# Optimization experiments

Measured on AMD Instinct MI355X. Metric: run time of the kernel, lower is better.

## Reference

```python
import jax, jax.numpy as jnp
import numpy as np

N, G, NPG = 8192, 128, 64        # total nodes, graphs, nodes per graph
D_IN, H, D_OUT = 128, 128, 10
DEG = 16                          # avg degree -> E = N*DEG
K = int(NPG * 0.5)                # keep_ratio = 0.5 -> topk per graph


def setup_inputs() -> dict:
    key = jax.random.key(0)
    ks = jax.random.split(key, 20)
    E = N * DEG
    # within-graph random edges (graphs are contiguous blocks of NPG nodes)
    src = jax.random.randint(ks[0], (E,), 0, NPG)
    dst = jax.random.randint(ks[1], (E,), 0, NPG)
    offs = jnp.repeat(jnp.arange(G, dtype=jnp.int32) * NPG, NPG * DEG)
    edge_index = jnp.stack([src.astype(jnp.int32) + offs, dst.astype(jnp.int32) + offs])
    batch = jnp.repeat(jnp.arange(G, dtype=jnp.int32), NPG)
    x = jax.random.normal(ks[2], (N, D_IN), jnp.float32)

    def lin(k, i, o):
        return jax.random.normal(k, (i, o), jnp.float32) * (1.0 / np.sqrt(i))

    return {
        "x": x, "edge_index": edge_index, "batch": batch,
        "W1": lin(ks[3], D_IN, H), "b1": jnp.zeros((H,), jnp.float32),
        "W2": lin(ks[4], H, H),    "b2": jnp.zeros((H,), jnp.float32),
        "W3": lin(ks[5], H, H),    "b3": jnp.zeros((H,), jnp.float32),
        "Wa": lin(ks[6], 3 * H, 1), "ba": jnp.zeros((1,), jnp.float32),
        "M1": lin(ks[7], 6 * H, H),      "c1": jnp.zeros((H,), jnp.float32),
        "M2": lin(ks[8], H, H // 2),     "c2": jnp.zeros((H // 2,), jnp.float32),
        "M3": lin(ks[9], H // 2, D_OUT), "c3": jnp.zeros((D_OUT,), jnp.float32),
    }


def reference(x, edge_index, batch, W1, b1, W2, b2, W3, b3, Wa, ba,
              M1, c1, M2, c2, M3, c3):
    n = x.shape[0]
    # generate_adjacency: dense [N,N] from edge list (symmetrized)
    A = jnp.zeros((n, n), x.dtype).at[edge_index[0], edge_index[1]].set(1.0)
    A = jnp.maximum(A, A.T)
    # normalize_adjacency: D^{-1/2} (A + I) D^{-1/2}
    A = A + jnp.eye(n, dtype=x.dtype)
    dinv = jax.lax.rsqrt(A.sum(axis=1))
    A = A * dinv[:, None] * dinv[None, :]

    gcn = lambda X, W, b: A @ (X @ W) + b
    h1 = jax.nn.relu(gcn(x, W1, b1))
    h2 = jax.nn.relu(gcn(h1, W2, b2))
    h3 = jax.nn.relu(gcn(h2, W3, b3))
    feats = jnp.concatenate([h1, h2, h3], axis=1)          # [N, 3H]

    # SelfAttentionPooling: GCN attention score + tanh + per-graph topk
    score = jnp.tanh((A @ (feats @ Wa) + ba)[:, 0])        # [N]
    s = score.reshape(G, NPG)                              # [G, NPG]
    _, idx = jax.lax.top_k(s, K)                           # [G, K]
    fg = feats.reshape(G, NPG, 3 * H)
    sel = jnp.take_along_axis(fg, idx[..., None], axis=1)  # [G, K, 3H]
    ssel = jnp.take_along_axis(s, idx, axis=1)             # [G, K]
    masked = sel * ssel[..., None]

    # Readout: mean || max per graph -> [G, 6H]
    readout = jnp.concatenate([masked.mean(axis=1), masked.max(axis=1)], axis=1)

    # MLP (dropout inactive at inference)
    h = jax.nn.relu(readout @ M1 + c1)
    h = jax.nn.relu(h @ M2 + c2)
    return h @ M3 + c3                                     # [G, D_OUT]
```

## Files before the change

kernel.cpp:

```cpp
#include <hip/hip_runtime.h>


#define NGRAPH 128
#define EPG    1024
#define ETOT   131072
#define DIM    128
#define KSEL   32
#define SA     68
#define SH     132

#define OFF_A   0
#define OFF_W   (64*SA)
#define OFF_T   (OFF_W + 16*DIM)
#define OFF_H1  (OFF_T  + 64*SH)
#define OFF_H2  (OFF_H1 + 64*SH)
#define OFF_H3  (OFF_H2 + 64*SH)
#define OFF_PRE (OFF_H3 + 64*SH)
#define OFF_SC  (OFF_PRE + 64)
#define OFF_SEL (OFF_SC + 64)
#define LDS_FLOATS (OFF_SEL + 64)
#define LDS_BYTES  (LDS_FLOATS * 4)

#define FMA8(A, xs, w0, w1) do { \
  A[0] += (xs)*(w0).x; A[1] += (xs)*(w0).y; A[2] += (xs)*(w0).z; A[3] += (xs)*(w0).w; \
  A[4] += (xs)*(w1).x; A[5] += (xs)*(w1).y; A[6] += (xs)*(w1).z; A[7] += (xs)*(w1).w; } while(0)

__device__ __forceinline__ void gcn_layer(float* lds, const float* IN, float* OUT,
                                          const float* __restrict__ Wg,
                                          const float* __restrict__ bg,
                                          const float* __restrict__ waCol, int tid)
{
  float* sW  = lds + OFF_W;
  float* sT  = lds + OFF_T;
  float* sA  = lds + OFF_A;
  float* pre = lds + OFF_PRE;
  const int rq = tid >> 4;
  const int cb = tid & 15;
  const int r0 = rq * 4;
  const int c0 = cb * 8;

  float acc[4][8];
  #pragma unroll
  for (int rr = 0; rr < 4; ++rr)
    #pragma unroll
    for (int cc = 0; cc < 8; ++cc) acc[rr][cc] = 0.f;

  for (int kc = 0; kc < 8; ++kc) {
    {
      const float4* wsrc = (const float4*)(Wg + kc * 16 * DIM);
      float4* wdst = (float4*)sW;
      wdst[tid]       = wsrc[tid];
      wdst[tid + 256] = wsrc[tid + 256];
    }
    __syncthreads();
    #pragma unroll
    for (int kt = 0; kt < 4; ++kt) {
      const int kl = kt * 4;
      const int kg = kc * 16 + kl;
      float4 xv[4];
      #pragma unroll
      for (int rr = 0; rr < 4; ++rr)
        xv[rr] = *(const float4*)&IN[(r0 + rr) * SH + kg];
      float4 w0[4], w1[4];
      #pragma unroll
      for (int i = 0; i < 4; ++i) {
        w0[i] = *(const float4*)&sW[(kl + i) * DIM + c0];
        w1[i] = *(const float4*)&sW[(kl + i) * DIM + c0 + 4];
      }
      #pragma unroll
      for (int rr = 0; rr < 4; ++rr) {
        FMA8(acc[rr], xv[rr].x, w0[0], w1[0]);
        FMA8(acc[rr], xv[rr].y, w0[1], w1[1]);
        FMA8(acc[rr], xv[rr].z, w0[2], w1[2]);
        FMA8(acc[rr], xv[rr].w, w0[3], w1[3]);
      }
    }
    __syncthreads();
  }
  #pragma unroll
  for (int rr = 0; rr < 4; ++rr) {
    float4 t0 = make_float4(acc[rr][0], acc[rr][1], acc[rr][2], acc[rr][3]);
    float4 t1 = make_float4(acc[rr][4], acc[rr][5], acc[rr][6], acc[rr][7]);
    *(float4*)&sT[(r0 + rr) * SH + c0]     = t0;
    *(float4*)&sT[(r0 + rr) * SH + c0 + 4] = t1;
  }
  __syncthreads();

  float4 bv0 = *(const float4*)&bg[c0];
  float4 bv1 = *(const float4*)&bg[c0 + 4];
  float a2[4][8];
  #pragma unroll
  for (int rr = 0; rr < 4; ++rr) {
    a2[rr][0] = bv0.x; a2[rr][1] = bv0.y; a2[rr][2] = bv0.z; a2[rr][3] = bv0.w;
    a2[rr][4] = bv1.x; a2[rr][5] = bv1.y; a2[rr][6] = bv1.z; a2[rr][7] = bv1.w;
  }
  for (int j = 0; j < 64; j += 4) {
    float4 av[4];
    #pragma unroll
    for (int rr = 0; rr < 4; ++rr)
      av[rr] = *(const float4*)&sA[(r0 + rr) * SA + j];
    float4 t0[4], t1[4];
    #pragma unroll
    for (int jj = 0; jj < 4; ++jj) {
      t0[jj] = *(const float4*)&sT[(j + jj) * SH + c0];
      t1[jj] = *(const float4*)&sT[(j + jj) * SH + c0 + 4];
    }
    #pragma unroll
    for (int rr = 0; rr < 4; ++rr) {
      FMA8(a2[rr], av[rr].x, t0[0], t1[0]);
      FMA8(a2[rr], av[rr].y, t0[1], t1[1]);
      FMA8(a2[rr], av[rr].z, t0[2], t1[2]);
      FMA8(a2[rr], av[rr].w, t0[3], t1[3]);
    }
  }
  float4 wa0 = *(const float4*)&waCol[c0];
  float4 wa1 = *(const float4*)&waCol[c0 + 4];
  float pp[4];
  #pragma unroll
  for (int rr = 0; rr < 4; ++rr) {
    float4 o0, o1;
    o0.x = fmaxf(a2[rr][0], 0.f); o0.y = fmaxf(a2[rr][1], 0.f);
    o0.z = fmaxf(a2[rr][2], 0.f); o0.w = fmaxf(a2[rr][3], 0.f);
    o1.x = fmaxf(a2[rr][4], 0.f); o1.y = fmaxf(a2[rr][5], 0.f);
    o1.z = fmaxf(a2[rr][6], 0.f); o1.w = fmaxf(a2[rr][7], 0.f);
    *(float4*)&OUT[(r0 + rr) * SH + c0]     = o0;
    *(float4*)&OUT[(r0 + rr) * SH + c0 + 4] = o1;
    pp[rr] = o0.x*wa0.x + o0.y*wa0.y + o0.z*wa0.z + o0.w*wa0.w
           + o1.x*wa1.x + o1.y*wa1.y + o1.z*wa1.z + o1.w*wa1.w;
  }
  #pragma unroll
  for (int rr = 0; rr < 4; ++rr) {
    pp[rr] += __shfl_xor(pp[rr], 1);
    pp[rr] += __shfl_xor(pp[rr], 2);
    pp[rr] += __shfl_xor(pp[rr], 4);
    pp[rr] += __shfl_xor(pp[rr], 8);
  }
  if ((tid & 15) == 0) {
    #pragma unroll
    for (int rr = 0; rr < 4; ++rr) pre[r0 + rr] += pp[rr];
  }
  __syncthreads();
}

extern "C" __global__ void __launch_bounds__(256, 1)
sagpool(const float* __restrict__ x,  const int* __restrict__ ei,
        const float* __restrict__ W1, const float* __restrict__ b1,
        const float* __restrict__ W2, const float* __restrict__ b2,
        const float* __restrict__ W3, const float* __restrict__ b3,
        const float* __restrict__ Wa, const float* __restrict__ ba,
        const float* __restrict__ M1, const float* __restrict__ c1,
        const float* __restrict__ M2, const float* __restrict__ c2,
        const float* __restrict__ M3, const float* __restrict__ c3,
        float* __restrict__ out)
{
  extern __shared__ float lds[];
  const int g   = blockIdx.x;
  const int tid = threadIdx.x;
  float* sA  = lds + OFF_A;
  float* pre = lds + OFF_PRE;
  float* sc  = lds + OFF_SC;
  float* sel = lds + OFF_SEL;

  for (int i = tid; i < 64 * SA; i += 256) sA[i] = 0.f;
  if (tid < 64) pre[tid] = 0.f;
  __syncthreads();
  {
    const int* srcp = ei + g * EPG;
    const int* dstp = ei + ETOT + g * EPG;
    #pragma unroll
    for (int t = 0; t < 4; ++t) {
      int e = tid + t * 256;
      int s = srcp[e] & 63;
      int d = dstp[e] & 63;
      sA[s * SA + d] = 1.0f;
      sA[d * SA + s] = 1.0f;
    }
  }
  __syncthreads();
  if (tid < 64) sA[tid * SA + tid] += 1.0f;
  __syncthreads();
  {
    int r = tid >> 2, q = tid & 3;
    float sum = 0.f;
    int jb = q * 16;
    #pragma unroll
    for (int j = 0; j < 16; ++j) sum += sA[r * SA + jb + j];
    sum += __shfl_xor(sum, 1);
    sum += __shfl_xor(sum, 2);
    if (q == 0) sc[r] = 1.0f / sqrtf(sum);
  }
  __syncthreads();
  for (int i = tid; i < 4096; i += 256) {
    int r = i >> 6, c = i & 63;
    sA[r * SA + c] *= sc[r] * sc[c];
  }
  {
    const float4* xg = (const float4*)(x + g * 64 * DIM);
    float* h3 = lds + OFF_H3;
    for (int i = tid; i < 2048; i += 256) {
      int r = i >> 5, c4 = i & 31;
      *(float4*)&h3[r * SH + c4 * 4] = xg[i];
    }
  }
  __syncthreads();

  gcn_layer(lds, lds + OFF_H3, lds + OFF_H1, W1, b1, Wa + 0,   tid);
  gcn_layer(lds, lds + OFF_H1, lds + OFF_H2, W2, b2, Wa + 128, tid);
  gcn_layer(lds, lds + OFF_H2, lds + OFF_H3, W3, b3, Wa + 256, tid);

  {
    int r = tid >> 2, q = tid & 3;
    float partial = 0.f;
    int jb = q * 16;
    #pragma unroll
    for (int j = 0; j < 16; ++j) partial += sA[r * SA + jb + j] * pre[jb + j];
    partial += __shfl_xor(partial, 1);
    partial += __shfl_xor(partial, 2);
    if (q == 0) sc[r] = tanhf(partial + ba[0]);
  }
  __syncthreads();

  if (tid < 64) {
    float mys = sc[tid];
    int cnt = 0;
    for (int j = 0; j < 64; ++j) {
      float sj = sc[j];
      cnt += (sj > mys || (sj == mys && j < tid)) ? 1 : 0;
    }
    sel[tid] = (cnt < KSEL) ? 1.0f : 0.0f;
  }
  __syncthreads();

  float* ro  = lds + OFF_T;
  float* mh  = lds + OFF_T + 768;
  float* hm  = lds + OFF_T + 1024;
  float* h2m = lds + OFF_T + 1152;
  for (int c = tid; c < 384; c += 256) {
    int which = c >> 7, cc = c & 127;
    const float* buf = (which == 0) ? (lds + OFF_H1)
                     : (which == 1) ? (lds + OFF_H2) : (lds + OFF_H3);
    float sum = 0.f, mx = -1e30f;
    for (int i = 0; i < 64; ++i) {
      if (sel[i] > 0.5f) {
        float v = sc[i] * buf[i * SH + cc];
        sum += v;
        mx = fmaxf(mx, v);
      }
    }
    ro[c]       = sum * (1.0f / KSEL);
    ro[384 + c] = mx;
  }
  __syncthreads();

  {
    int j = tid & 127, half = tid >> 7;
    float acc = 0.f;
    int k0 = half * 384;
    for (int k = k0; k < k0 + 384; k += 4) {
      float4 r4 = *(const float4*)&ro[k];
      acc += r4.x * M1[(k + 0) * DIM + j];
      acc += r4.y * M1[(k + 1) * DIM + j];
      acc += r4.z * M1[(k + 2) * DIM + j];
      acc += r4.w * M1[(k + 3) * DIM + j];
    }
    mh[half * 128 + j] = acc;
  }
  __syncthreads();
  if (tid < 128) hm[tid] = fmaxf(mh[tid] + mh[128 + tid] + c1[tid], 0.f);
  __syncthreads();
  if (tid < 64) {
    float acc = c2[tid];
    for (int k = 0; k < 128; ++k) acc += hm[k] * M2[k * 64 + tid];
    h2m[tid] = fmaxf(acc, 0.f);
  }
  __syncthreads();
  if (tid < 10) {
    float acc = c3[tid];
    for (int k = 0; k < 64; ++k) acc += h2m[k] * M3[k * 10 + tid];
    out[g * 10 + tid] = acc;
  }
}

extern "C" void kernel_launch(void* const* d_in, const int* in_sizes, int n_in,
                              void* d_out, int out_size, void* d_ws, size_t ws_size,
                              hipStream_t stream) {
  const float* x  = (const float*)d_in[0];
  const int*   ei = (const int*)d_in[1];
  const float* W1 = (const float*)d_in[3];
  const float* b1 = (const float*)d_in[4];
  const float* W2 = (const float*)d_in[5];
  const float* b2 = (const float*)d_in[6];
  const float* W3 = (const float*)d_in[7];
  const float* b3 = (const float*)d_in[8];
  const float* Wa = (const float*)d_in[9];
  const float* ba = (const float*)d_in[10];
  const float* M1 = (const float*)d_in[11];
  const float* c1 = (const float*)d_in[12];
  const float* M2 = (const float*)d_in[13];
  const float* c2 = (const float*)d_in[14];
  const float* M3 = (const float*)d_in[15];
  const float* c3 = (const float*)d_in[16];
  float* out = (float*)d_out;

  (void)hipFuncSetAttribute(reinterpret_cast<const void*>(sagpool),
                            hipFuncAttributeMaxDynamicSharedMemorySize, LDS_BYTES);
  sagpool<<<NGRAPH, 256, LDS_BYTES, stream>>>(x, ei, W1, b1, W2, b2, W3, b3,
                                              Wa, ba, M1, c1, M2, c2, M3, c3, out);
}
```

Before: 157.6 us.

## Split monolithic per-graph kernel into multi-kernel pipeline with half-graph blocks

Replaces the single 128-block kernel with five launches: adjacency build plus X@W1 in parallel blocks, three fused GCN-layer kernels that each use two blocks per graph (32 rows each) and also compute the next layer's H@W, and a final pooling/MLP kernel. The intent is to fill more of the GPU's compute units than 128 blocks can and to shrink per-block LDS so more work runs concurrently. In exchange it adds launch overhead and round trips of intermediates through global workspace memory, and it applies a swizzled LDS layout to reduce bank conflicts.

```diff
diff --git a/kernel.cpp b/kernel.cpp
--- a/kernel.cpp
+++ b/kernel.cpp
@@ -7,164 +7,38 @@
 #define DIM    128
 #define KSEL   32
 #define SA     68
-#define SH     132
-
-#define OFF_A   0
-#define OFF_W   (64*SA)
-#define OFF_T   (OFF_W + 16*DIM)
-#define OFF_H1  (OFF_T  + 64*SH)
-#define OFF_H2  (OFF_H1 + 64*SH)
-#define OFF_H3  (OFF_H2 + 64*SH)
-#define OFF_PRE (OFF_H3 + 64*SH)
-#define OFF_SC  (OFF_PRE + 64)
-#define OFF_SEL (OFF_SC + 64)
-#define LDS_FLOATS (OFF_SEL + 64)
-#define LDS_BYTES  (LDS_FLOATS * 4)
+
+#define WS_A   0
+#define WS_T1  524288
+#define WS_T2  (WS_T1 + 1048576)
+#define WS_H1  (WS_T2 + 1048576)
+#define WS_H2  (WS_H1 + 1048576)
+#define WS_H3  (WS_H2 + 1048576)
+#define WS_PRE (WS_H3 + 1048576)
+#define WS_T3  WS_T1
+
+__device__ __forceinline__ int swoff(int k, int o) {
+  return k * 140 + o * 8 + ((o >> 2) << 2);
+}
 
 #define FMA8(A, xs, w0, w1) do { \
   A[0] += (xs)*(w0).x; A[1] += (xs)*(w0).y; A[2] += (xs)*(w0).z; A[3] += (xs)*(w0).w; \
   A[4] += (xs)*(w1).x; A[5] += (xs)*(w1).y; A[6] += (xs)*(w1).z; A[7] += (xs)*(w1).w; } while(0)
 
-__device__ __forceinline__ void gcn_layer(float* lds, const float* IN, float* OUT,
-                                          const float* __restrict__ Wg,
-                                          const float* __restrict__ bg,
-                                          const float* __restrict__ waCol, int tid)
+__global__ void __launch_bounds__(256, 1)
+k_adj_xw(const int* __restrict__ ei, const float* __restrict__ x,
+         const float* __restrict__ W1, float* __restrict__ wsA,
+         float* __restrict__ T1)
 {
-  float* sW  = lds + OFF_W;
-  float* sT  = lds + OFF_T;
-  float* sA  = lds + OFF_A;
-  float* pre = lds + OFF_PRE;
-  const int rq = tid >> 4;
-  const int cb = tid & 15;
-  const int r0 = rq * 4;
-  const int c0 = cb * 8;
-
-  float acc[4][8];
-  #pragma unroll
-  for (int rr = 0; rr < 4; ++rr)
-    #pragma unroll
-    for (int cc = 0; cc < 8; ++cc) acc[rr][cc] = 0.f;
-
-  for (int kc = 0; kc < 8; ++kc) {
-    {
-      const float4* wsrc = (const float4*)(Wg + kc * 16 * DIM);
-      float4* wdst = (float4*)sW;
-      wdst[tid]       = wsrc[tid];
-      wdst[tid + 256] = wsrc[tid + 256];
-    }
+  __shared__ float smem[6464];
+  const int tid = threadIdx.x;
+
+  if (blockIdx.x < NGRAPH) {
+    const int g = blockIdx.x;
+    float* sA = smem;
+    float* dv = smem + 64 * SA;
+    for (int i = tid; i < 64 * SA; i += 256) sA[i] = 0.f;
     __syncthreads();
-    #pragma unroll
-    for (int kt = 0; kt < 4; ++kt) {
-      const int kl = kt * 4;
-      const int kg = kc * 16 + kl;
-      float4 xv[4];
-      #pragma unroll
-      for (int rr = 0; rr < 4; ++rr)
-        xv[rr] = *(const float4*)&IN[(r0 + rr) * SH + kg];
-      float4 w0[4], w1[4];
-      #pragma unroll
-      for (int i = 0; i < 4; ++i) {
-        w0[i] = *(const float4*)&sW[(kl + i) * DIM + c0];
-        w1[i] = *(const float4*)&sW[(kl + i) * DIM + c0 + 4];
-      }
-      #pragma unroll
-      for (int rr = 0; rr < 4; ++rr) {
-        FMA8(acc[rr], xv[rr].x, w0[0], w1[0]);
-        FMA8(acc[rr], xv[rr].y, w0[1], w1[1]);
-        FMA8(acc[rr], xv[rr].z, w0[2], w1[2]);
-        FMA8(acc[rr], xv[rr].w, w0[3], w1[3]);
-      }
-    }
-    __syncthreads();
-  }
-  #pragma unroll
-  for (int rr = 0; rr < 4; ++rr) {
-    float4 t0 = make_float4(acc[rr][0], acc[rr][1], acc[rr][2], acc[rr][3]);
-    float4 t1 = make_float4(acc[rr][4], acc[rr][5], acc[rr][6], acc[rr][7]);
-    *(float4*)&sT[(r0 + rr) * SH + c0]     = t0;
-    *(float4*)&sT[(r0 + rr) * SH + c0 + 4] = t1;
-  }
-  __syncthreads();
-
-  float4 bv0 = *(const float4*)&bg[c0];
-  float4 bv1 = *(const float4*)&bg[c0 + 4];
-  float a2[4][8];
-  #pragma unroll
-  for (int rr = 0; rr < 4; ++rr) {
-    a2[rr][0] = bv0.x; a2[rr][1] = bv0.y; a2[rr][2] = bv0.z; a2[rr][3] = bv0.w;
-    a2[rr][4] = bv1.x; a2[rr][5] = bv1.y; a2[rr][6] = bv1.z; a2[rr][7] = bv1.w;
-  }
-  for (int j = 0; j < 64; j += 4) {
-    float4 av[4];
-    #pragma unroll
-    for (int rr = 0; rr < 4; ++rr)
-      av[rr] = *(const float4*)&sA[(r0 + rr) * SA + j];
-    float4 t0[4], t1[4];
-    #pragma unroll
-    for (int jj = 0; jj < 4; ++jj) {
-      t0[jj] = *(const float4*)&sT[(j + jj) * SH + c0];
-      t1[jj] = *(const float4*)&sT[(j + jj) * SH + c0 + 4];
-    }
-    #pragma unroll
-    for (int rr = 0; rr < 4; ++rr) {
-      FMA8(a2[rr], av[rr].x, t0[0], t1[0]);
-      FMA8(a2[rr], av[rr].y, t0[1], t1[1]);
-      FMA8(a2[rr], av[rr].z, t0[2], t1[2]);
-      FMA8(a2[rr], av[rr].w, t0[3], t1[3]);
-    }
-  }
-  float4 wa0 = *(const float4*)&waCol[c0];
-  float4 wa1 = *(const float4*)&waCol[c0 + 4];
-  float pp[4];
-  #pragma unroll
-  for (int rr = 0; rr < 4; ++rr) {
-    float4 o0, o1;
-    o0.x = fmaxf(a2[rr][0], 0.f); o0.y = fmaxf(a2[rr][1], 0.f);
-    o0.z = fmaxf(a2[rr][2], 0.f); o0.w = fmaxf(a2[rr][3], 0.f);
-    o1.x = fmaxf(a2[rr][4], 0.f); o1.y = fmaxf(a2[rr][5], 0.f);
-    o1.z = fmaxf(a2[rr][6], 0.f); o1.w = fmaxf(a2[rr][7], 0.f);
-    *(float4*)&OUT[(r0 + rr) * SH + c0]     = o0;
-    *(float4*)&OUT[(r0 + rr) * SH + c0 + 4] = o1;
-    pp[rr] = o0.x*wa0.x + o0.y*wa0.y + o0.z*wa0.z + o0.w*wa0.w
-           + o1.x*wa1.x + o1.y*wa1.y + o1.z*wa1.z + o1.w*wa1.w;
-  }
-  #pragma unroll
-  for (int rr = 0; rr < 4; ++rr) {
-    pp[rr] += __shfl_xor(pp[rr], 1);
-    pp[rr] += __shfl_xor(pp[rr], 2);
-    pp[rr] += __shfl_xor(pp[rr], 4);
-    pp[rr] += __shfl_xor(pp[rr], 8);
-  }
-  if ((tid & 15) == 0) {
-    #pragma unroll
-    for (int rr = 0; rr < 4; ++rr) pre[r0 + rr] += pp[rr];
-  }
-  __syncthreads();
-}
-
-extern "C" __global__ void __launch_bounds__(256, 1)
-sagpool(const float* __restrict__ x,  const int* __restrict__ ei,
-        const float* __restrict__ W1, const float* __restrict__ b1,
-        const float* __restrict__ W2, const float* __restrict__ b2,
-        const float* __restrict__ W3, const float* __restrict__ b3,
-        const float* __restrict__ Wa, const float* __restrict__ ba,
-        const float* __restrict__ M1, const float* __restrict__ c1,
-        const float* __restrict__ M2, const float* __restrict__ c2,
-        const float* __restrict__ M3, const float* __restrict__ c3,
-        float* __restrict__ out)
-{
-  extern __shared__ float lds[];
-  const int g   = blockIdx.x;
-  const int tid = threadIdx.x;
-  float* sA  = lds + OFF_A;
-  float* pre = lds + OFF_PRE;
-  float* sc  = lds + OFF_SC;
-  float* sel = lds + OFF_SEL;
-
-  for (int i = tid; i < 64 * SA; i += 256) sA[i] = 0.f;
-  if (tid < 64) pre[tid] = 0.f;
-  __syncthreads();
-  {
     const int* srcp = ei + g * EPG;
     const int* dstp = ei + ETOT + g * EPG;
     #pragma unroll
@@ -175,74 +49,262 @@
       sA[s * SA + d] = 1.0f;
       sA[d * SA + s] = 1.0f;
     }
-  }
-  __syncthreads();
-  if (tid < 64) sA[tid * SA + tid] += 1.0f;
+    __syncthreads();
+    if (tid < 64) sA[tid * SA + tid] += 1.0f;
+    __syncthreads();
+    {
+      int r = tid >> 2, q = tid & 3;
+      float sum = 0.f;
+      int jb = q * 16;
+      #pragma unroll
+      for (int j = 0; j < 16; ++j) sum += sA[r * SA + jb + j];
+      sum += __shfl_xor(sum, 1);
+      sum += __shfl_xor(sum, 2);
+      if (q == 0) dv[r] = 1.0f / sqrtf(sum);
+    }
+    __syncthreads();
+    float* outA = wsA + g * 4096;
+    for (int i = tid; i < 4096; i += 256) {
+      int r = i >> 6, c = i & 63;
+      outA[i] = sA[r * SA + c] * dv[r] * dv[c];
+    }
+  } else {
+    const int row0 = (blockIdx.x - NGRAPH) * 32;
+    float* sX = smem;
+    float* sW = smem + 4224;
+    {
+      const float4* src = (const float4*)(x + row0 * DIM);
+      for (int i = tid; i < 1024; i += 256) {
+        int r = i >> 5, q = i & 31;
+        *(float4*)&sX[r * 132 + q * 4] = src[i];
+      }
+    }
+    const int rg = tid >> 4, cg = tid & 15;
+    const int r0 = rg * 2, c0 = cg * 8;
+    float acc[2][8];
+    #pragma unroll
+    for (int rr = 0; rr < 2; ++rr)
+      #pragma unroll
+      for (int cc = 0; cc < 8; ++cc) acc[rr][cc] = 0.f;
+
+    for (int kc = 0; kc < 8; ++kc) {
+      __syncthreads();
+      const float4* wsrc = (const float4*)(W1 + kc * 16 * DIM);
+      for (int i = tid; i < 512; i += 256) {
+        int k = i >> 5, q = i & 31;
+        *(float4*)&sW[swoff(k, q >> 1) + (q & 1) * 4] = wsrc[i];
+      }
+      __syncthreads();
+      #pragma unroll
+      for (int kq = 0; kq < 4; ++kq) {
+        const int kk = kq * 4, kg = kc * 16 + kk;
+        float4 x0 = *(const float4*)&sX[r0 * 132 + kg];
+        float4 x1 = *(const float4*)&sX[(r0 + 1) * 132 + kg];
+        float4 w0[4], w1[4];
+        #pragma unroll
+        for (int j = 0; j < 4; ++j) {
+          int base = swoff(kk + j, cg);
+          w0[j] = *(const float4*)&sW[base];
+          w1[j] = *(const float4*)&sW[base + 4];
+        }
+        FMA8(acc[0], x0.x, w0[0], w1[0]); FMA8(acc[0], x0.y, w0[1], w1[1]);
+        FMA8(acc[0], x0.z, w0[2], w1[2]); FMA8(acc[0], x0.w, w0[3], w1[3]);
+        FMA8(acc[1], x1.x, w0[0], w1[0]); FMA8(acc[1], x1.y, w0[1], w1[1]);
+        FMA8(acc[1], x1.z, w0[2], w1[2]); FMA8(acc[1], x1.w, w0[3], w1[3]);
+      }
+    }
+    #pragma unroll
+    for (int rr = 0; rr < 2; ++rr) {
+      float4 t0 = make_float4(acc[rr][0], acc[rr][1], acc[rr][2], acc[rr][3]);
+      float4 t1 = make_float4(acc[rr][4], acc[rr][5], acc[rr][6], acc[rr][7]);
+      *(float4*)&T1[(row0 + r0 + rr) * DIM + c0]     = t0;
+      *(float4*)&T1[(row0 + r0 + rr) * DIM + c0 + 4] = t1;
+    }
+  }
+}
+
+#define FOFF_A 8960
+#define FOFF_H 11136
+#define FOFF_W 15360
+#define FUSED_LDS_FLOATS 17600
+#define FUSED_LDS_BYTES (FUSED_LDS_FLOATS * 4)
+
+__global__ void __launch_bounds__(256, 1)
+k_fused(const float* __restrict__ Tin, const float* __restrict__ wsA,
+        const float* __restrict__ bg, const float* __restrict__ waCol,
+        const float* __restrict__ Wn, float* __restrict__ Hout,
+        float* __restrict__ Tout, float* __restrict__ pre,
+        const int first, const int do_xw)
+{
+  extern __shared__ float lds[];
+  float* sT  = lds;
+  float* sAl = lds + FOFF_A;
+  float* sh  = lds + FOFF_H;
+  float* sW  = lds + FOFF_W;
+  const int tid = threadIdx.x;
+  const int g = blockIdx.x >> 1;
+  const int rbase = (blockIdx.x & 1) * 32;
+  const int growbase = g * 64 + rbase;
+
+  {
+    const float4* src = (const float4*)(Tin + g * 64 * DIM);
+    for (int i = tid; i < 2048; i += 256) {
+      int k = i >> 5, q = i & 31;
+      *(float4*)&sT[swoff(k, q >> 1) + (q & 1) * 4] = src[i];
+    }
+    const float* asrc = wsA + g * 4096 + rbase * 64;
+    for (int i = tid; i < 2048; i += 256)
+      sAl[(i >> 6) * SA + (i & 63)] = asrc[i];
+  }
+  __syncthreads();
+
+  const int rg = tid >> 4, cg = tid & 15;
+  const int r0 = rg * 2, c0 = cg * 8;
+
+  float4 bv0 = *(const float4*)&bg[c0];
+  float4 bv1 = *(const float4*)&bg[c0 + 4];
+  float acc[2][8];
+  #pragma unroll
+  for (int rr = 0; rr < 2; ++rr) {
+    acc[rr][0] = bv0.x; acc[rr][1] = bv0.y; acc[rr][2] = bv0.z; acc[rr][3] = bv0.w;
+    acc[rr][4] = bv1.x; acc[rr][5] = bv1.y; acc[rr][6] = bv1.z; acc[rr][7] = bv1.w;
+  }
+  #pragma unroll
+  for (int kq = 0; kq < 16; ++kq) {
+    const int kk = kq * 4;
+    float4 a0 = *(const float4*)&sAl[r0 * SA + kk];
+    float4 a1 = *(const float4*)&sAl[(r0 + 1) * SA + kk];
+    float4 t0[4], t1[4];
+    #pragma unroll
+    for (int j = 0; j < 4; ++j) {
+      int base = swoff(kk + j, cg);
+      t0[j] = *(const float4*)&sT[base];
+      t1[j] = *(const float4*)&sT[base + 4];
+    }
+    FMA8(acc[0], a0.x, t0[0], t1[0]); FMA8(acc[0], a0.y, t0[1], t1[1]);
+    FMA8(acc[0], a0.z, t0[2], t1[2]); FMA8(acc[0], a0.w, t0[3], t1[3]);
+    FMA8(acc[1], a1.x, t0[0], t1[0]); FMA8(acc[1], a1.y, t0[1], t1[1]);
+    FMA8(acc[1], a1.z, t0[2], t1[2]); FMA8(acc[1], a1.w, t0[3], t1[3]);
+  }
+  float4 wa0 = *(const float4*)&waCol[c0];
+  float4 wa1 = *(const float4*)&waCol[c0 + 4];
+  float pp[2];
+  #pragma unroll
+  for (int rr = 0; rr < 2; ++rr) {
+    float4 o0, o1;
+    o0.x = fmaxf(acc[rr][0], 0.f); o0.y = fmaxf(acc[rr][1], 0.f);
+    o0.z = fmaxf(acc[rr][2], 0.f); o0.w = fmaxf(acc[rr][3], 0.f);
+    o1.x = fmaxf(acc[rr][4], 0.f); o1.y = fmaxf(acc[rr][5], 0.f);
+    o1.z = fmaxf(acc[rr][6], 0.f); o1.w = fmaxf(acc[rr][7], 0.f);
+    *(float4*)&sh[(r0 + rr) * 132 + c0]     = o0;
+    *(float4*)&sh[(r0 + rr) * 132 + c0 + 4] = o1;
+    *(float4*)&Hout[(growbase + r0 + rr) * DIM + c0]     = o0;
+    *(float4*)&Hout[(growbase + r0 + rr) * DIM + c0 + 4] = o1;
+    pp[rr] = o0.x*wa0.x + o0.y*wa0.y + o0.z*wa0.z + o0.w*wa0.w
+           + o1.x*wa1.x + o1.y*wa1.y + o1.z*wa1.z + o1.w*wa1.w;
+  }
+  #pragma unroll
+  for (int rr = 0; rr < 2; ++rr) {
+    pp[rr] += __shfl_xor(pp[rr], 1);
+    pp[rr] += __shfl_xor(pp[rr], 2);
+    pp[rr] += __shfl_xor(pp[rr], 4);
+    pp[rr] += __shfl_xor(pp[rr], 8);
+  }
+  if (cg == 0) {
+    #pragma unroll
+    for (int rr = 0; rr < 2; ++rr) {
+      int row = growbase + r0 + rr;
+      if (first) pre[row] = pp[rr];
+      else       pre[row] += pp[rr];
+    }
+  }
+
+  if (do_xw) {
+    float acc2[2][8];
+    #pragma unroll
+    for (int rr = 0; rr < 2; ++rr)
+      #pragma unroll
+      for (int cc = 0; cc < 8; ++cc) acc2[rr][cc] = 0.f;
+    for (int kc = 0; kc < 8; ++kc) {
+      __syncthreads();
+      const float4* wsrc = (const float4*)(Wn + kc * 16 * DIM);
+      for (int i = tid; i < 512; i += 256) {
+        int k = i >> 5, q = i & 31;
+        *(float4*)&sW[swoff(k, q >> 1) + (q & 1) * 4] = wsrc[i];
+      }
+      __syncthreads();
+      #pragma unroll
+      for (int kq = 0; kq < 4; ++kq) {
+        const int kk = kq * 4, kg = kc * 16 + kk;
+        float4 h0 = *(const float4*)&sh[r0 * 132 + kg];
+        float4 h1 = *(const float4*)&sh[(r0 + 1) * 132 + kg];
+        float4 w0[4], w1[4];
+        #pragma unroll
+        for (int j = 0; j < 4; ++j) {
+          int base = swoff(kk + j, cg);
+          w0[j] = *(const float4*)&sW[base];
+          w1[j] = *(const float4*)&sW[base + 4];
+        }
+        FMA8(acc2[0], h0.x, w0[0], w1[0]); FMA8(acc2[0], h0.y, w0[1], w1[1]);
+        FMA8(acc2[0], h0.z, w0[2], w1[2]); FMA8(acc2[0], h0.w, w0[3], w1[3]);
+        FMA8(acc2[1], h1.x, w0[0], w1[0]); FMA8(acc2[1], h1.y, w0[1], w1[1]);
+        FMA8(acc2[1], h1.z, w0[2], w1[2]); FMA8(acc2[1], h1.w, w0[3], w1[3]);
+      }
+    }
+    #pragma unroll
+    for (int rr = 0; rr < 2; ++rr) {
+      float4 t0 = make_float4(acc2[rr][0], acc2[rr][1], acc2[rr][2], acc2[rr][3]);
+      float4 t1 = make_float4(acc2[rr][4], acc2[rr][5], acc2[rr][6], acc2[rr][7]);
+      *(float4*)&Tout[(growbase + r0 + rr) * DIM + c0]     = t0;
+      *(float4*)&Tout[(growbase + r0 + rr) * DIM + c0 + 4] = t1;
+    }
+  }
+}
+
+__global__ void __launch_bounds__(256, 1)
+k_final(const float* __restrict__ wsA, const float* __restrict__ pre,
+        const float* __restrict__ h1g, const float* __restrict__ h2g,
+        const float* __restrict__ h3g, const float* __restrict__ ba,
+        const float* __restrict__ M1, const float* __restrict__ c1,
+        const float* __restrict__ M2, const float* __restrict__ c2,
+        const float* __restrict__ M3, const float* __restrict__ c3,
+        float* __restrict__ out)
+{
+  __shared__ float spre[64], ssc[64], ssel[64];
+  __shared__ float ro[768], mh[256], hm[128], h2m[64];
+  const int g = blockIdx.x, tid = threadIdx.x;
+
+  if (tid < 64) spre[tid] = pre[g * 64 + tid];
   __syncthreads();
   {
     int r = tid >> 2, q = tid & 3;
-    float sum = 0.f;
-    int jb = q * 16;
-    #pragma unroll
-    for (int j = 0; j < 16; ++j) sum += sA[r * SA + jb + j];
-    sum += __shfl_xor(sum, 1);
-    sum += __shfl_xor(sum, 2);
-    if (q == 0) sc[r] = 1.0f / sqrtf(sum);
-  }
-  __syncthreads();
-  for (int i = tid; i < 4096; i += 256) {
-    int r = i >> 6, c = i & 63;
-    sA[r * SA + c] *= sc[r] * sc[c];
-  }
-  {
-    const float4* xg = (const float4*)(x + g * 64 * DIM);
-    float* h3 = lds + OFF_H3;
-    for (int i = tid; i < 2048; i += 256) {
-      int r = i >> 5, c4 = i & 31;
-      *(float4*)&h3[r * SH + c4 * 4] = xg[i];
-    }
-  }
-  __syncthreads();
-
-  gcn_layer(lds, lds + OFF_H3, lds + OFF_H1, W1, b1, Wa + 0,   tid);
-  gcn_layer(lds, lds + OFF_H1, lds + OFF_H2, W2, b2, Wa + 128, tid);
-  gcn_layer(lds, lds + OFF_H2, lds + OFF_H3, W3, b3, Wa + 256, tid);
-
-  {
-    int r = tid >> 2, q = tid & 3;
+    const float* Ar = wsA + g * 4096 + r * 64;
     float partial = 0.f;
     int jb = q * 16;
     #pragma unroll
-    for (int j = 0; j < 16; ++j) partial += sA[r * SA + jb + j] * pre[jb + j];
+    for (int j = 0; j < 16; ++j) partial += Ar[jb + j] * spre[jb + j];
     partial += __shfl_xor(partial, 1);
     partial += __shfl_xor(partial, 2);
-    if (q == 0) sc[r] = tanhf(partial + ba[0]);
-  }
-  __syncthreads();
-
+    if (q == 0) ssc[r] = tanhf(partial + ba[0]);
+  }
+  __syncthreads();
   if (tid < 64) {
-    float mys = sc[tid];
+    float mys = ssc[tid];
     int cnt = 0;
     for (int j = 0; j < 64; ++j) {
-      float sj = sc[j];
+      float sj = ssc[j];
       cnt += (sj > mys || (sj == mys && j < tid)) ? 1 : 0;
     }
-    sel[tid] = (cnt < KSEL) ? 1.0f : 0.0f;
-  }
-  __syncthreads();
-
-  float* ro  = lds + OFF_T;
-  float* mh  = lds + OFF_T + 768;
-  float* hm  = lds + OFF_T + 1024;
-  float* h2m = lds + OFF_T + 1152;
+    ssel[tid] = (cnt < KSEL) ? 1.0f : 0.0f;
+  }
+  __syncthreads();
   for (int c = tid; c < 384; c += 256) {
     int which = c >> 7, cc = c & 127;
-    const float* buf = (which == 0) ? (lds + OFF_H1)
-                     : (which == 1) ? (lds + OFF_H2) : (lds + OFF_H3);
+    const float* hb = ((which == 0) ? h1g : (which == 1) ? h2g : h3g) + g * 64 * DIM;
     float sum = 0.f, mx = -1e30f;
     for (int i = 0; i < 64; ++i) {
-      if (sel[i] > 0.5f) {
-        float v = sc[i] * buf[i * SH + cc];
+      if (ssel[i] > 0.5f) {
+        float v = ssc[i] * hb[i * DIM + cc];
         sum += v;
         mx = fmaxf(mx, v);
       }
@@ -251,7 +313,6 @@
     ro[384 + c] = mx;
   }
   __syncthreads();
-
   {
     int j = tid & 127, half = tid >> 7;
     float acc = 0.f;
@@ -302,8 +363,23 @@
   const float* c3 = (const float*)d_in[16];
   float* out = (float*)d_out;
 
-  (void)hipFuncSetAttribute(reinterpret_cast<const void*>(sagpool),
-                            hipFuncAttributeMaxDynamicSharedMemorySize, LDS_BYTES);
-  sagpool<<<NGRAPH, 256, LDS_BYTES, stream>>>(x, ei, W1, b1, W2, b2, W3, b3,
-                                              Wa, ba, M1, c1, M2, c2, M3, c3, out);
-}
+  float* ws  = (float*)d_ws;
+  float* wsA = ws + WS_A;
+  float* T1  = ws + WS_T1;
+  float* T2  = ws + WS_T2;
+  float* T3  = ws + WS_T3;
+  float* H1  = ws + WS_H1;
+  float* H2  = ws + WS_H2;
+  float* H3  = ws + WS_H3;
+  float* pre = ws + WS_PRE;
+
+  (void)hipFuncSetAttribute(reinterpret_cast<const void*>(k_fused),
+                            hipFuncAttributeMaxDynamicSharedMemorySize, FUSED_LDS_BYTES);
+
+  k_adj_xw<<<NGRAPH + 256, 256, 0, stream>>>(ei, x, W1, wsA, T1);
+  k_fused<<<256, 256, FUSED_LDS_BYTES, stream>>>(T1, wsA, b1, Wa,           W2, H1, T2, pre, 1, 1);
+  k_fused<<<256, 256, FUSED_LDS_BYTES, stream>>>(T2, wsA, b2, Wa + DIM,     W3, H2, T3, pre, 0, 1);
+  k_fused<<<256, 256, FUSED_LDS_BYTES, stream>>>(T3, wsA, b3, Wa + 2 * DIM, W3, H3, T2, pre, 0, 0);
+  k_final<<<NGRAPH, 256, 0, stream>>>(wsA, pre, H1, H2, H3, ba,
+                                      M1, c1, M2, c2, M3, c3, out);
+}
```

Measured after the change: 178.9 us. 13.6% more time.

## Spill layer activations to global workspace and shrink LDS footprint

Applied to the files above, without the earlier changes.

Per-layer GCN outputs are no longer kept as three separate LDS buffers. Each layer now writes its ReLU output to a global workspace and reuses a single LDS buffer in place, with an extra barrier before the overwrite. The LDS rows use a padded, swizzled layout (stride 140 with a pad every 32 columns) to cut bank conflicts. The readout reads the activations back from global memory. The aim is a smaller LDS footprint and fewer bank conflicts; the cost is extra global traffic and an added sync, and launch_bounds is dropped.

```diff
diff --git a/kernel.cpp b/kernel.cpp
--- a/kernel.cpp
+++ b/kernel.cpp
@@ -7,33 +7,38 @@
 #define DIM    128
 #define KSEL   32
 #define SA     68
-#define SH     132
-
-#define OFF_A   0
-#define OFF_W   (64*SA)
-#define OFF_T   (OFF_W + 16*DIM)
-#define OFF_H1  (OFF_T  + 64*SH)
-#define OFF_H2  (OFF_H1 + 64*SH)
-#define OFF_H3  (OFF_H2 + 64*SH)
-#define OFF_PRE (OFF_H3 + 64*SH)
-#define OFF_SC  (OFF_PRE + 64)
-#define OFF_SEL (OFF_SC + 64)
-#define LDS_FLOATS (OFF_SEL + 64)
+#define SWT    140
+
+__device__ __forceinline__ int woff(int k, int c) {
+  return k * SWT + c + ((c >> 5) << 2);
+}
+
+#define O_A    0
+#define O_B0   4352
+#define O_W    13312
+#define O_PRE  15552
+#define O_SC   15616
+#define O_SEL  15680
+#define LDS_FLOATS 15744
 #define LDS_BYTES  (LDS_FLOATS * 4)
+#define O_RO   O_W
+#define O_MH   (O_W + 768)
+#define O_HM   (O_W + 1024)
+#define O_H2M  (O_W + 1152)
 
 #define FMA8(A, xs, w0, w1) do { \
   A[0] += (xs)*(w0).x; A[1] += (xs)*(w0).y; A[2] += (xs)*(w0).z; A[3] += (xs)*(w0).w; \
   A[4] += (xs)*(w1).x; A[5] += (xs)*(w1).y; A[6] += (xs)*(w1).z; A[7] += (xs)*(w1).w; } while(0)
 
-__device__ __forceinline__ void gcn_layer(float* lds, const float* IN, float* OUT,
-                                          const float* __restrict__ Wg,
-                                          const float* __restrict__ bg,
-                                          const float* __restrict__ waCol, int tid)
+__device__ void gcn_layer(float* lds, const float* __restrict__ Wg,
+                          const float* __restrict__ bg,
+                          const float* __restrict__ waCol,
+                          float* __restrict__ Hg, int tid)
 {
-  float* sW  = lds + OFF_W;
-  float* sT  = lds + OFF_T;
-  float* sA  = lds + OFF_A;
-  float* pre = lds + OFF_PRE;
+  float* sA  = lds + O_A;
+  float* B0  = lds + O_B0;
+  float* sW  = lds + O_W;
+  float* pre = lds + O_PRE;
   const int rq = tid >> 4;
   const int cb = tid & 15;
   const int r0 = rq * 4;
@@ -47,10 +52,10 @@
 
   for (int kc = 0; kc < 8; ++kc) {
     {
-      const float4* wsrc = (const float4*)(Wg + kc * 16 * DIM);
-      float4* wdst = (float4*)sW;
-      wdst[tid]       = wsrc[tid];
-      wdst[tid + 256] = wsrc[tid + 256];
+      const float4* src = (const float4*)(Wg + kc * 16 * DIM);
+      int i0 = tid, i1 = tid + 256;
+      *(float4*)&sW[woff(i0 >> 5, (i0 & 31) * 4)] = src[i0];
+      *(float4*)&sW[woff(i1 >> 5, (i1 & 31) * 4)] = src[i1];
     }
     __syncthreads();
     #pragma unroll
@@ -60,12 +65,13 @@
       float4 xv[4];
       #pragma unroll
       for (int rr = 0; rr < 4; ++rr)
-        xv[rr] = *(const float4*)&IN[(r0 + rr) * SH + kg];
+        xv[rr] = *(const float4*)&B0[woff(r0 + rr, kg)];
       float4 w0[4], w1[4];
       #pragma unroll
       for (int i = 0; i < 4; ++i) {
-        w0[i] = *(const float4*)&sW[(kl + i) * DIM + c0];
-        w1[i] = *(const float4*)&sW[(kl + i) * DIM + c0 + 4];
+        int base = woff(kl + i, c0);
+        w0[i] = *(const float4*)&sW[base];
+        w1[i] = *(const float4*)&sW[base + 4];
       }
       #pragma unroll
       for (int rr = 0; rr < 4; ++rr) {
@@ -79,10 +85,9 @@
   }
   #pragma unroll
   for (int rr = 0; rr < 4; ++rr) {
-    float4 t0 = make_float4(acc[rr][0], acc[rr][1], acc[rr][2], acc[rr][3]);
-    float4 t1 = make_float4(acc[rr][4], acc[rr][5], acc[rr][6], acc[rr][7]);
-    *(float4*)&sT[(r0 + rr) * SH + c0]     = t0;
-    *(float4*)&sT[(r0 + rr) * SH + c0 + 4] = t1;
+    int base = woff(r0 + rr, c0);
+    *(float4*)&B0[base]     = make_float4(acc[rr][0], acc[rr][1], acc[rr][2], acc[rr][3]);
+    *(float4*)&B0[base + 4] = make_float4(acc[rr][4], acc[rr][5], acc[rr][6], acc[rr][7]);
   }
   __syncthreads();
 
@@ -102,8 +107,9 @@
     float4 t0[4], t1[4];
     #pragma unroll
     for (int jj = 0; jj < 4; ++jj) {
-      t0[jj] = *(const float4*)&sT[(j + jj) * SH + c0];
-      t1[jj] = *(const float4*)&sT[(j + jj) * SH + c0 + 4];
+      int base = woff(j + jj, c0);
+      t0[jj] = *(const float4*)&B0[base];
+      t1[jj] = *(const float4*)&B0[base + 4];
     }
     #pragma unroll
     for (int rr = 0; rr < 4; ++rr) {
@@ -115,18 +121,25 @@
   }
   float4 wa0 = *(const float4*)&waCol[c0];
   float4 wa1 = *(const float4*)&waCol[c0 + 4];
+  float4 o0[4], o1[4];
   float pp[4];
   #pragma unroll
   for (int rr = 0; rr < 4; ++rr) {
-    float4 o0, o1;
-    o0.x = fmaxf(a2[rr][0], 0.f); o0.y = fmaxf(a2[rr][1], 0.f);
-    o0.z = fmaxf(a2[rr][2], 0.f); o0.w = fmaxf(a2[rr][3], 0.f);
-    o1.x = fmaxf(a2[rr][4], 0.f); o1.y = fmaxf(a2[rr][5], 0.f);
-    o1.z = fmaxf(a2[rr][6], 0.f); o1.w = fmaxf(a2[rr][7], 0.f);
-    *(float4*)&OUT[(r0 + rr) * SH + c0]     = o0;
-    *(float4*)&OUT[(r0 + rr) * SH + c0 + 4] = o1;
-    pp[rr] = o0.x*wa0.x + o0.y*wa0.y + o0.z*wa0.z + o0.w*wa0.w
-           + o1.x*wa1.x + o1.y*wa1.y + o1.z*wa1.z + o1.w*wa1.w;
+    o0[rr].x = fmaxf(a2[rr][0], 0.f); o0[rr].y = fmaxf(a2[rr][1], 0.f);
+    o0[rr].z = fmaxf(a2[rr][2], 0.f); o0[rr].w = fmaxf(a2[rr][3], 0.f);
+    o1[rr].x = fmaxf(a2[rr][4], 0.f); o1[rr].y = fmaxf(a2[rr][5], 0.f);
+    o1[rr].z = fmaxf(a2[rr][6], 0.f); o1[rr].w = fmaxf(a2[rr][7], 0.f);
+    pp[rr] = o0[rr].x*wa0.x + o0[rr].y*wa0.y + o0[rr].z*wa0.z + o0[rr].w*wa0.w
+           + o1[rr].x*wa1.x + o1[rr].y*wa1.y + o1[rr].z*wa1.z + o1[rr].w*wa1.w;
+  }
+  __syncthreads();
+  #pragma unroll
+  for (int rr = 0; rr < 4; ++rr) {
+    int base = woff(r0 + rr, c0);
+    *(float4*)&B0[base]     = o0[rr];
+    *(float4*)&B0[base + 4] = o1[rr];
+    *(float4*)&Hg[(r0 + rr) * DIM + c0]     = o0[rr];
+    *(float4*)&Hg[(r0 + rr) * DIM + c0 + 4] = o1[rr];
   }
   #pragma unroll
   for (int rr = 0; rr < 4; ++rr) {
@@ -135,14 +148,14 @@
     pp[rr] += __shfl_xor(pp[rr], 4);
     pp[rr] += __shfl_xor(pp[rr], 8);
   }
-  if ((tid & 15) == 0) {
+  if (cb == 0) {
     #pragma unroll
     for (int rr = 0; rr < 4; ++rr) pre[r0 + rr] += pp[rr];
   }
   __syncthreads();
 }
 
-extern "C" __global__ void __launch_bounds__(256, 1)
+extern "C" __global__ void
 sagpool(const float* __restrict__ x,  const int* __restrict__ ei,
         const float* __restrict__ W1, const float* __restrict__ b1,
         const float* __restrict__ W2, const float* __restrict__ b2,
@@ -151,15 +164,20 @@
         const float* __restrict__ M1, const float* __restrict__ c1,
         const float* __restrict__ M2, const float* __restrict__ c2,
         const float* __restrict__ M3, const float* __restrict__ c3,
-        float* __restrict__ out)
+        float* __restrict__ h1w, float* __restrict__ h2w,
+        float* __restrict__ h3w, float* __restrict__ out)
 {
   extern __shared__ float lds[];
-  const int g   = blockIdx.x;
-  const int tid = threadIdx.x;
-  float* sA  = lds + OFF_A;
-  float* pre = lds + OFF_PRE;
-  float* sc  = lds + OFF_SC;
-  float* sel = lds + OFF_SEL;
+  const int g = blockIdx.x, tid = threadIdx.x;
+  float* sA  = lds + O_A;
+  float* B0  = lds + O_B0;
+  float* pre = lds + O_PRE;
+  float* sc  = lds + O_SC;
+  float* sel = lds + O_SEL;
+  float* ro  = lds + O_RO;
+  float* mh  = lds + O_MH;
+  float* hm  = lds + O_HM;
+  float* h2m = lds + O_H2M;
 
   for (int i = tid; i < 64 * SA; i += 256) sA[i] = 0.f;
   if (tid < 64) pre[tid] = 0.f;
@@ -196,27 +214,24 @@
   }
   {
     const float4* xg = (const float4*)(x + g * 64 * DIM);
-    float* h3 = lds + OFF_H3;
-    for (int i = tid; i < 2048; i += 256) {
-      int r = i >> 5, c4 = i & 31;
-      *(float4*)&h3[r * SH + c4 * 4] = xg[i];
-    }
-  }
-  __syncthreads();
-
-  gcn_layer(lds, lds + OFF_H3, lds + OFF_H1, W1, b1, Wa + 0,   tid);
-  gcn_layer(lds, lds + OFF_H1, lds + OFF_H2, W2, b2, Wa + 128, tid);
-  gcn_layer(lds, lds + OFF_H2, lds + OFF_H3, W3, b3, Wa + 256, tid);
+    for (int i = tid; i < 2048; i += 256)
+      *(float4*)&B0[woff(i >> 5, (i & 31) * 4)] = xg[i];
+  }
+  __syncthreads();
+
+  gcn_layer(lds, W1, b1, Wa,           h1w + g * 8192, tid);
+  gcn_layer(lds, W2, b2, Wa + DIM,     h2w + g * 8192, tid);
+  gcn_layer(lds, W3, b3, Wa + 2 * DIM, h3w + g * 8192, tid);
 
   {
     int r = tid >> 2, q = tid & 3;
-    float partial = 0.f;
+    float p = 0.f;
     int jb = q * 16;
     #pragma unroll
-    for (int j = 0; j < 16; ++j) partial += sA[r * SA + jb + j] * pre[jb + j];
-    partial += __shfl_xor(partial, 1);
-    partial += __shfl_xor(partial, 2);
-    if (q == 0) sc[r] = tanhf(partial + ba[0]);
+    for (int j = 0; j < 16; ++j) p += sA[r * SA + jb + j] * pre[jb + j];
+    p += __shfl_xor(p, 1);
+    p += __shfl_xor(p, 2);
+    if (q == 0) sc[r] = tanhf(p + ba[0]);
   }
   __syncthreads();
 
@@ -231,18 +246,13 @@
   }
   __syncthreads();
 
-  float* ro  = lds + OFF_T;
-  float* mh  = lds + OFF_T + 768;
-  float* hm  = lds + OFF_T + 1024;
-  float* h2m = lds + OFF_T + 1152;
   for (int c = tid; c < 384; c += 256) {
     int which = c >> 7, cc = c & 127;
-    const float* buf = (which == 0) ? (lds + OFF_H1)
-                     : (which == 1) ? (lds + OFF_H2) : (lds + OFF_H3);
+    const float* hb = ((which == 0) ? h1w : (which == 1) ? h2w : h3w) + g * 8192;
     float sum = 0.f, mx = -1e30f;
     for (int i = 0; i < 64; ++i) {
       if (sel[i] > 0.5f) {
-        float v = sc[i] * buf[i * SH + cc];
+        float v = sc[i] * hb[i * DIM + cc];
         sum += v;
         mx = fmaxf(mx, v);
       }
@@ -254,30 +264,30 @@
 
   {
     int j = tid & 127, half = tid >> 7;
-    float acc = 0.f;
+    float a = 0.f;
     int k0 = half * 384;
     for (int k = k0; k < k0 + 384; k += 4) {
       float4 r4 = *(const float4*)&ro[k];
-      acc += r4.x * M1[(k + 0) * DIM + j];
-      acc += r4.y * M1[(k + 1) * DIM + j];
-      acc += r4.z * M1[(k + 2) * DIM + j];
-      acc += r4.w * M1[(k + 3) * DIM + j];
-    }
-    mh[half * 128 + j] = acc;
+      a += r4.x * M1[(k + 0) * DIM + j];
+      a += r4.y * M1[(k + 1) * DIM + j];
+      a += r4.z * M1[(k + 2) * DIM + j];
+      a += r4.w * M1[(k + 3) * DIM + j];
+    }
+    mh[half * 128 + j] = a;
   }
   __syncthreads();
   if (tid < 128) hm[tid] = fmaxf(mh[tid] + mh[128 + tid] + c1[tid], 0.f);
   __syncthreads();
   if (tid < 64) {
-    float acc = c2[tid];
-    for (int k = 0; k < 128; ++k) acc += hm[k] * M2[k * 64 + tid];
-    h2m[tid] = fmaxf(acc, 0.f);
+    float a = c2[tid];
+    for (int k = 0; k < 128; ++k) a += hm[k] * M2[k * 64 + tid];
+    h2m[tid] = fmaxf(a, 0.f);
   }
   __syncthreads();
   if (tid < 10) {
-    float acc = c3[tid];
-    for (int k = 0; k < 64; ++k) acc += h2m[k] * M3[k * 10 + tid];
-    out[g * 10 + tid] = acc;
+    float a = c3[tid];
+    for (int k = 0; k < 64; ++k) a += h2m[k] * M3[k * 10 + tid];
+    out[g * 10 + tid] = a;
   }
 }
 
@@ -302,8 +312,14 @@
   const float* c3 = (const float*)d_in[16];
   float* out = (float*)d_out;
 
+  float* ws  = (float*)d_ws;
+  float* h1w = ws;
+  float* h2w = ws + 1048576;
+  float* h3w = ws + 2097152;
+
   (void)hipFuncSetAttribute(reinterpret_cast<const void*>(sagpool),
                             hipFuncAttributeMaxDynamicSharedMemorySize, LDS_BYTES);
   sagpool<<<NGRAPH, 256, LDS_BYTES, stream>>>(x, ei, W1, b1, W2, b2, W3, b3,
-                                              Wa, ba, M1, c1, M2, c2, M3, c3, out);
+                                              Wa, ba, M1, c1, M2, c2, M3, c3,
+                                              h1w, h2w, h3w, out);
 }
```

Result: slower. 168.3 us (+6.8%).
